# Kernel tuning notes

Measured on AMD Instinct MI355X. Metric: run time of the kernel, lower is better.

## Reference

```python
import jax, jax.numpy as jnp
import numpy as np

B, S, D_MODEL, D_KEY = 4, 2048, 1024, 128


def setup_inputs() -> dict:
    key = jax.random.key(0)
    kq, kk, kv, kwq, kwk, kwv = jax.random.split(key, 6)
    queries = jax.random.normal(kq, (B, S, D_MODEL), dtype=jnp.float32)
    keys = jax.random.normal(kk, (B, S, D_MODEL), dtype=jnp.float32)
    values = jax.random.normal(kv, (B, S, D_MODEL), dtype=jnp.float32)
    # causal mask: 1 where attention is allowed (j <= i), 0 otherwise
    mask = jnp.broadcast_to(jnp.tril(jnp.ones((S, S), dtype=jnp.int32)), (B, S, S))
    # torch nn.Linear weights are [out, in]; init ~ U(-1/sqrt(in), 1/sqrt(in))
    bound = 1.0 / np.sqrt(D_MODEL)
    Wq = jax.random.uniform(kwq, (D_KEY, D_MODEL), jnp.float32, -bound, bound)
    Wk = jax.random.uniform(kwk, (D_KEY, D_MODEL), jnp.float32, -bound, bound)
    Wv = jax.random.uniform(kwv, (D_KEY, D_MODEL), jnp.float32, -bound, bound)
    return {"queries": queries, "keys": keys, "values": values, "mask": mask,
            "Wq": Wq, "Wk": Wk, "Wv": Wv}


def reference(queries, keys, values, mask, Wq, Wk, Wv):
    d_key = Wq.shape[0]
    q = jnp.einsum('bsd,kd->bsk', queries, Wq)   # [B,S,d_key]
    k = jnp.einsum('bsd,kd->bsk', keys, Wk)
    v = jnp.einsum('bsd,kd->bsk', values, Wv)
    attn = jnp.einsum('bqk,bsk->bqs', q, k) / jnp.sqrt(jnp.float32(d_key))  # [B,S,S]
    attn = jnp.where(mask == 0, -jnp.inf, attn)
    attn = jax.nn.softmax(attn, axis=-1)
    return jnp.einsum('bqs,bsk->bqk', attn, v)   # [B,S,d_key]
```

## Files before the change

kernel.cpp:

```cpp
#include <hip/hip_runtime.h>
#include <hip/hip_bf16.h>

#define NB 4
#define SEQ 2048
#define DMODEL 1024
#define DKEY 128

using f32x4  = __attribute__((ext_vector_type(4))) float;
using bf16x8 = __attribute__((ext_vector_type(8))) short;
using u16x4  = __attribute__((ext_vector_type(4))) unsigned short;
using u16x8  = __attribute__((ext_vector_type(8))) unsigned short;

__device__ __forceinline__ unsigned short f2bf(float f) {
  __hip_bfloat16 h = __float2bfloat16(f);
  return __builtin_bit_cast(unsigned short, h);
}
__device__ __forceinline__ bf16x8 pack8(f32x4 lo, f32x4 hi) {
  u16x8 p = { f2bf(lo[0]), f2bf(lo[1]), f2bf(lo[2]), f2bf(lo[3]),
              f2bf(hi[0]), f2bf(hi[1]), f2bf(hi[2]), f2bf(hi[3]) };
  return __builtin_bit_cast(bf16x8, p);
}
__device__ __forceinline__ void gload16(const void* g, void* l) {
  __builtin_amdgcn_global_load_lds(
      (const __attribute__((address_space(1))) void*)g,
      (__attribute__((address_space(3))) void*)l, 16, 0, 0);
}

__global__ __launch_bounds__(256) void wconv_kernel(
    const float* __restrict__ Wq, const float* __restrict__ Wk,
    const float* __restrict__ Wv, unsigned short* __restrict__ Wb)
{
  int id = blockIdx.x * 256 + threadIdx.x;
  const float* src = (id < 16384) ? Wq : (id < 32768) ? Wk : Wv;
  int off = (id & 16383) * 8;
  float4 a = *reinterpret_cast<const float4*>(&src[off]);
  float4 b = *reinterpret_cast<const float4*>(&src[off + 4]);
  u16x8 p = { f2bf(a.x), f2bf(a.y), f2bf(a.z), f2bf(a.w),
              f2bf(b.x), f2bf(b.y), f2bf(b.z), f2bf(b.w) };
  *reinterpret_cast<u16x8*>(&Wb[(size_t)(id >> 14) * 131072 + off]) = p;
}

__global__ __launch_bounds__(256, 2) void proj_kernel(
    const float* __restrict__ Xq, const float* __restrict__ Xk, const float* __restrict__ Xv,
    const unsigned short* __restrict__ Wb,
    unsigned short* __restrict__ Yq, unsigned short* __restrict__ Yk,
    unsigned short* __restrict__ Vt)
{
  const int z = blockIdx.z;
  const float* X = (z == 0) ? Xq : (z == 1) ? Xk : Xv;
  const unsigned short* W = Wb + (size_t)z * 131072;

  __shared__ alignas(16) float          XL[4][64 * 32];
  __shared__ alignas(16) unsigned short WL[4][128 * 32];

  const int t     = threadIdx.x;
  const int lane  = t & 63;
  const int w     = t >> 6;
  const int lr    = lane & 15;
  const int hi    = lane >> 4;
  const int rbase = hi * 4;
  const long m0   = (long)blockIdx.x * 64;

  const int xg_row[2] = { (0 * 256 + t) >> 3, (1 * 256 + t) >> 3 };
  const int xg_col[2] = { ((((0 * 256 + t) & 7) ^ (xg_row[0] & 7)) << 2),
                          ((((1 * 256 + t) & 7) ^ (xg_row[1] & 7)) << 2) };
  const int wg_row[2] = { (0 * 256 + t) >> 2, (1 * 256 + t) >> 2 };
  const int wg_col[2] = { ((((0 * 256 + t) & 3) ^ (wg_row[0] & 3)) << 3),
                          ((((1 * 256 + t) & 3) ^ (wg_row[1] & 3)) << 3) };

#define PJ_ISSUE(ks) do {                                                     \
    const int _b = (ks) & 3;                                                  \
    _Pragma("unroll")                                                         \
    for (int i = 0; i < 2; ++i) {                                             \
      gload16(&X[(m0 + xg_row[i]) * (long)DMODEL + (ks) * 32 + xg_col[i]],    \
              &XL[_b][(i * 256 + w * 64) * 4]);                               \
      gload16(&W[(size_t)wg_row[i] * DMODEL + (ks) * 32 + wg_col[i]],         \
              &WL[_b][(i * 256 + w * 64) * 8]);                               \
    }                                                                         \
  } while (0)

  f32x4 acc[8];
  const f32x4 zero = {0.f, 0.f, 0.f, 0.f};
#pragma unroll
  for (int n = 0; n < 8; ++n) acc[n] = zero;

  PJ_ISSUE(0);
  PJ_ISSUE(1);
  PJ_ISSUE(2);

  const int arow = w * 16 + lr;
  for (int ks = 0; ks < 32; ++ks) {
    if (ks < 30)       asm volatile("s_waitcnt vmcnt(8)" ::: "memory");
    else if (ks == 30) asm volatile("s_waitcnt vmcnt(4)" ::: "memory");
    else               asm volatile("s_waitcnt vmcnt(0)" ::: "memory");
    __builtin_amdgcn_s_barrier();
    if (ks + 3 < 32) PJ_ISSUE(ks + 3);

    const int buf = ks & 3;
    const float* xrow = &XL[buf][arow * 32];
    f32x4 xlo = *reinterpret_cast<const f32x4*>(xrow + (((hi * 2)     ^ (lr & 7)) << 2));
    f32x4 xhi = *reinterpret_cast<const f32x4*>(xrow + (((hi * 2 + 1) ^ (lr & 7)) << 2));
    bf16x8 a = pack8(xlo, xhi);
#pragma unroll
    for (int n = 0; n < 8; ++n) {
      const int wrow = n * 16 + lr;
      bf16x8 b = *reinterpret_cast<const bf16x8*>(
          &WL[buf][wrow * 32 + ((hi ^ (wrow & 3)) << 3)]);
      acc[n] = __builtin_amdgcn_mfma_f32_16x16x32_bf16(a, b, acc[n], 0, 0, 0);
    }
  }
#undef PJ_ISSUE

  if (z != 2) {
    unsigned short* Y = (z == 0) ? Yq : Yk;
#pragma unroll
    for (int n = 0; n < 8; ++n)
#pragma unroll
      for (int r = 0; r < 4; ++r) {
        long row = m0 + w * 16 + rbase + r;
        Y[row * DKEY + n * 16 + lr] = f2bf(acc[n][r]);
      }
  } else {
    unsigned short* Tl = reinterpret_cast<unsigned short*>(&XL[0][0]);
    __syncthreads();
#pragma unroll
    for (int n = 0; n < 8; ++n)
#pragma unroll
      for (int r = 0; r < 4; ++r)
        Tl[(n * 16 + lr) * 72 + (w * 16 + rbase + r)] = f2bf(acc[n][r]);
    __syncthreads();
    const int bb = (int)(m0 >> 11);
    const int s0 = (int)(m0 & 2047);
#pragma unroll
    for (int i = 0; i < 4; ++i) {
      int id = t + 256 * i;
      int dr = id >> 3;
      int c8 = (id & 7) << 3;
      u16x8 v = *reinterpret_cast<const u16x8*>(&Tl[dr * 72 + c8]);
      *reinterpret_cast<u16x8*>(&Vt[((size_t)bb * DKEY + dr) * SEQ + s0 + c8]) = v;
    }
  }
}

__global__ __launch_bounds__(512, 2) void attn_kernel(
    const unsigned short* __restrict__ Q,
    const unsigned short* __restrict__ K,
    const unsigned short* __restrict__ Vt,
    float* __restrict__ O)
{
  const int  L    = blockIdx.x;
  const int  b    = (L & 7) >> 1;
  const int  qt   = 63 - (((L >> 3) << 1) | (L & 1));
  const int  q0   = qt * 32;
  const long base = (long)b * SEQ;
  const int  nt   = (q0 >> 6) + 1;
  const int  nsteps = (nt + 3) >> 2;

  __shared__ alignas(16) unsigned short Kl[4][64][128];
  __shared__ alignas(16) unsigned short Vl[4][128][64];
  __shared__ alignas(16) unsigned short Plds[8][16][72];
  __shared__ float Sm[4][32], Sl[4][32];

  const int t     = threadIdx.x;
  const int lane  = t & 63;
  const int w     = t >> 6;
  const int g     = w >> 1;
  const int wq    = w & 1;
  const int lr    = lane & 15;
  const int hi    = lane >> 4;
  const int lk    = hi * 8;
  const int rbase = hi * 4;

  bf16x8 qa[4];
  {
    const long qrow = (base + q0 + wq * 16 + lr) * (long)DKEY;
#pragma unroll
    for (int dk = 0; dk < 4; ++dk)
      qa[dk] = *reinterpret_cast<const bf16x8*>(&Q[qrow + dk * 32 + lk]);
  }

  const f32x4 zero = {0.f, 0.f, 0.f, 0.f};
  f32x4 oacc[8];
#pragma unroll
  for (int n = 0; n < 8; ++n) oacc[n] = zero;
  float m_run[4], l_run[4];
#pragma unroll
  for (int r = 0; r < 4; ++r) { m_run[r] = -1e30f; l_run[r] = 0.0f; }

  const float sc = 0.08838834764831845f;
  const unsigned short* VtB = Vt + (size_t)b * DKEY * SEQ;

  for (int st = 0; st < nsteps; ++st) {
    const int kt  = st * 4 + g;
    const bool act = kt < nt;
    const int kv0 = kt * 64;

    if (act) {
      const unsigned short* Kp = K + (base + kv0) * (long)DKEY;
#pragma unroll
      for (int it = 0; it < 8; ++it) {
        int c = it * 128 + wq * 64 + lane;
        int row = c >> 4, sl = (c & 15) ^ (row & 7);
        *reinterpret_cast<u16x8*>(&Kl[g][row][sl * 8]) =
            *reinterpret_cast<const u16x8*>(&Kp[(size_t)c * 8]);
      }
#pragma unroll
      for (int it = 0; it < 8; ++it) {
        int c = it * 128 + wq * 64 + lane;
        int d = c >> 3, sl = c & 7, slp = sl ^ (d & 7);
        *reinterpret_cast<u16x8*>(&Vl[g][d][slp * 8]) =
            *reinterpret_cast<const u16x8*>(&VtB[(size_t)d * SEQ + kv0 + sl * 8]);
      }
    }
    __syncthreads();

    if (act) {
      f32x4 s[4];
#pragma unroll
      for (int kc = 0; kc < 4; ++kc) {
        s[kc] = zero;
#pragma unroll
        for (int dk = 0; dk < 4; ++dk) {
          bf16x8 kb = *reinterpret_cast<const bf16x8*>(
              &Kl[g][kc * 16 + lr][((dk * 4 + hi) ^ (lr & 7)) * 8]);
          s[kc] = __builtin_amdgcn_mfma_f32_16x16x32_bf16(qa[dk], kb, s[kc], 0, 0, 0);
        }
      }

      const bool dmask = (kt == nt - 1);
      float x[4][4];
#pragma unroll
      for (int kc = 0; kc < 4; ++kc)
#pragma unroll
        for (int r = 0; r < 4; ++r) {
          float xv = s[kc][r] * sc;
          if (dmask) {
            int col  = kv0 + kc * 16 + lr;
            int rowq = q0 + wq * 16 + rbase + r;
            if (col > rowq) xv = -1e30f;
          }
          x[kc][r] = xv;
        }

#pragma unroll
      for (int r = 0; r < 4; ++r) {
        float tm = fmaxf(fmaxf(x[0][r], x[1][r]), fmaxf(x[2][r], x[3][r]));
        tm = fmaxf(tm, __shfl_xor(tm, 1));
        tm = fmaxf(tm, __shfl_xor(tm, 2));
        tm = fmaxf(tm, __shfl_xor(tm, 4));
        tm = fmaxf(tm, __shfl_xor(tm, 8));
        float mnew = fmaxf(m_run[r], tm);
        float scl  = __expf(m_run[r] - mnew);
        m_run[r] = mnew;
        float ps = 0.0f;
#pragma unroll
        for (int kc = 0; kc < 4; ++kc) {
          float pp = __expf(x[kc][r] - mnew);
          ps += pp;
          Plds[w][rbase + r][kc * 16 + lr] = f2bf(pp);
        }
        ps += __shfl_xor(ps, 1);
        ps += __shfl_xor(ps, 2);
        ps += __shfl_xor(ps, 4);
        ps += __shfl_xor(ps, 8);
        l_run[r] = l_run[r] * scl + ps;
#pragma unroll
        for (int n = 0; n < 8; ++n) oacc[n][r] *= scl;
      }

#pragma unroll
      for (int kk = 0; kk < 2; ++kk) {
        bf16x8 pa = *reinterpret_cast<const bf16x8*>(&Plds[w][lr][kk * 32 + lk]);
#pragma unroll
        for (int n = 0; n < 8; ++n) {
          bf16x8 vb = *reinterpret_cast<const bf16x8*>(
              &Vl[g][n * 16 + lr][((kk * 4 + hi) ^ (lr & 7)) * 8]);
          oacc[n] = __builtin_amdgcn_mfma_f32_16x16x32_bf16(pa, vb, oacc[n], 0, 0, 0);
        }
      }
    }
    __syncthreads();
  }

  float* Om = reinterpret_cast<float*>(&Kl[0][0][0]);
#pragma unroll
  for (int n = 0; n < 8; ++n)
#pragma unroll
    for (int r = 0; r < 4; ++r)
      Om[(g * 32 + wq * 16 + rbase + r) * 128 + n * 16 + lr] = oacc[n][r];
  if (lr == 0) {
#pragma unroll
    for (int r = 0; r < 4; ++r) {
      Sm[g][wq * 16 + rbase + r] = m_run[r];
      Sl[g][wq * 16 + rbase + r] = l_run[r];
    }
  }
  __syncthreads();

  const int row = t >> 4;
  const int c0  = (t & 15) * 8;
  float mM = fmaxf(fmaxf(Sm[0][row], Sm[1][row]), fmaxf(Sm[2][row], Sm[3][row]));
  float wts[4], lsum = 0.0f;
#pragma unroll
  for (int gv = 0; gv < 4; ++gv) {
    wts[gv] = __expf(Sm[gv][row] - mM);
    lsum += wts[gv] * Sl[gv][row];
  }
  const float linv = 1.0f / lsum;
  f32x4 o0 = zero, o1 = zero;
#pragma unroll
  for (int gv = 0; gv < 4; ++gv) {
    const float* src = &Om[(gv * 32 + row) * 128 + c0];
    f32x4 a0 = *reinterpret_cast<const f32x4*>(src);
    f32x4 a1 = *reinterpret_cast<const f32x4*>(src + 4);
    const float wt = wts[gv];
#pragma unroll
    for (int j = 0; j < 4; ++j) { o0[j] += wt * a0[j]; o1[j] += wt * a1[j]; }
  }
#pragma unroll
  for (int j = 0; j < 4; ++j) { o0[j] *= linv; o1[j] *= linv; }
  float* op = &O[(base + q0 + row) * (long)DKEY + c0];
  *reinterpret_cast<f32x4*>(op)     = o0;
  *reinterpret_cast<f32x4*>(op + 4) = o1;
}

extern "C" void kernel_launch(void* const* d_in, const int* in_sizes, int n_in,
                              void* d_out, int out_size, void* d_ws, size_t ws_size,
                              hipStream_t stream) {
  const float* Xq = (const float*)d_in[0];
  const float* Xk = (const float*)d_in[1];
  const float* Xv = (const float*)d_in[2];
  const float* Wq = (const float*)d_in[4];
  const float* Wk = (const float*)d_in[5];
  const float* Wv = (const float*)d_in[6];

  unsigned short* qp  = (unsigned short*)d_ws;
  unsigned short* kp  = qp + (size_t)NB * SEQ * DKEY;
  unsigned short* vtp = kp + (size_t)NB * SEQ * DKEY;
  unsigned short* wbp = (unsigned short*)d_out;

  hipLaunchKernelGGL(wconv_kernel, dim3(192), dim3(256), 0, stream,
                     Wq, Wk, Wv, wbp);
  dim3 g1(SEQ * NB / 64, 1, 3);
  hipLaunchKernelGGL(proj_kernel, g1, dim3(256), 0, stream,
                     Xq, Xk, Xv, wbp, qp, kp, vtp);
  hipLaunchKernelGGL(attn_kernel, dim3(256), dim3(512), 0, stream,
                     qp, kp, vtp, (float*)d_out);
}
```

Before: 68.37 us.

## Stage projection X tile as bf16 in LDS in two halves, double-buffer W

The projection kernel now loads half of the 64-row X tile (512 columns) through registers, converts it to bf16 once, and stores it swizzled in LDS, instead of streaming fp32 X through a 4-deep async global-to-LDS pipeline and converting at every k-step. W keeps async loads but with a 2-stage buffer. This removes the repeated per-step fp32-to-bf16 packing and halves LDS bytes per X element. In exchange, X loads are synchronous bulk phases with no overlap against MFMA work, and an extra barrier is added per step.

```diff
diff --git a/kernel.cpp b/kernel.cpp
--- a/kernel.cpp
+++ b/kernel.cpp
@@ -14,11 +14,6 @@
 __device__ __forceinline__ unsigned short f2bf(float f) {
   __hip_bfloat16 h = __float2bfloat16(f);
   return __builtin_bit_cast(unsigned short, h);
-}
-__device__ __forceinline__ bf16x8 pack8(f32x4 lo, f32x4 hi) {
-  u16x8 p = { f2bf(lo[0]), f2bf(lo[1]), f2bf(lo[2]), f2bf(lo[3]),
-              f2bf(hi[0]), f2bf(hi[1]), f2bf(hi[2]), f2bf(hi[3]) };
-  return __builtin_bit_cast(bf16x8, p);
 }
 __device__ __forceinline__ void gload16(const void* g, void* l) {
   __builtin_amdgcn_global_load_lds(
@@ -50,8 +45,8 @@
   const float* X = (z == 0) ? Xq : (z == 1) ? Xk : Xv;
   const unsigned short* W = Wb + (size_t)z * 131072;
 
-  __shared__ alignas(16) float          XL[4][64 * 32];
-  __shared__ alignas(16) unsigned short WL[4][128 * 32];
+  __shared__ alignas(16) unsigned short XL[64 * 512];
+  __shared__ alignas(16) unsigned short WL[2][128 * 32];
 
   const int t     = threadIdx.x;
   const int lane  = t & 63;
@@ -60,56 +55,81 @@
   const int hi    = lane >> 4;
   const int rbase = hi * 4;
   const long m0   = (long)blockIdx.x * 64;
-
-  const int xg_row[2] = { (0 * 256 + t) >> 3, (1 * 256 + t) >> 3 };
-  const int xg_col[2] = { ((((0 * 256 + t) & 7) ^ (xg_row[0] & 7)) << 2),
-                          ((((1 * 256 + t) & 7) ^ (xg_row[1] & 7)) << 2) };
+  const int arow  = w * 16 + lr;
+
   const int wg_row[2] = { (0 * 256 + t) >> 2, (1 * 256 + t) >> 2 };
   const int wg_col[2] = { ((((0 * 256 + t) & 3) ^ (wg_row[0] & 3)) << 3),
                           ((((1 * 256 + t) & 3) ^ (wg_row[1] & 3)) << 3) };
 
-#define PJ_ISSUE(ks) do {                                                     \
-    const int _b = (ks) & 3;                                                  \
+#define W_ISSUE(ks) do {                                                      \
+    const int _s = (ks) & 1;                                                  \
     _Pragma("unroll")                                                         \
-    for (int i = 0; i < 2; ++i) {                                             \
-      gload16(&X[(m0 + xg_row[i]) * (long)DMODEL + (ks) * 32 + xg_col[i]],    \
-              &XL[_b][(i * 256 + w * 64) * 4]);                               \
+    for (int i = 0; i < 2; ++i)                                               \
       gload16(&W[(size_t)wg_row[i] * DMODEL + (ks) * 32 + wg_col[i]],         \
-              &WL[_b][(i * 256 + w * 64) * 8]);                               \
+              &WL[_s][(i * 256 + w * 64) * 8]);                               \
+  } while (0)
+
+#define P1_LOAD(cbase) do {                                                   \
+    for (int jb = 0; jb < 8; ++jb) {                                          \
+      float4 v[4];                                                            \
+      _Pragma("unroll")                                                       \
+      for (int u = 0; u < 4; ++u) {                                           \
+        int f = (jb * 4 + u) * 256 + t;                                       \
+        int row = f >> 7, c4 = (f & 127) << 2;                                \
+        v[u] = *reinterpret_cast<const float4*>(                              \
+            &X[(m0 + row) * (long)DMODEL + (cbase) + c4]);                    \
+      }                                                                       \
+      _Pragma("unroll")                                                       \
+      for (int u = 0; u < 4; ++u) {                                           \
+        int f = (jb * 4 + u) * 256 + t;                                       \
+        int row = f >> 7, c4 = (f & 127) << 2;                                \
+        u16x4 p = { f2bf(v[u].x), f2bf(v[u].y), f2bf(v[u].z), f2bf(v[u].w) }; \
+        *reinterpret_cast<u16x4*>(                                            \
+            &XL[row * 512 + (((c4 >> 3) ^ (row & 7)) << 3)                    \
+                + ((c4 >> 2) & 1) * 4]) = p;                                  \
+      }                                                                       \
     }                                                                         \
   } while (0)
 
+#define PJ_STEP(gks) do {                                                     \
+    if ((gks) < 31) asm volatile("s_waitcnt vmcnt(2)" ::: "memory");          \
+    else            asm volatile("s_waitcnt vmcnt(0)" ::: "memory");          \
+    __builtin_amdgcn_s_barrier();                                             \
+    {                                                                         \
+      const int _s  = (gks) & 1;                                              \
+      const int _gr = ((gks) & 15) * 4 + hi;                                  \
+      bf16x8 a = *reinterpret_cast<const bf16x8*>(                            \
+          &XL[arow * 512 + ((_gr ^ (lr & 7)) << 3)]);                         \
+      _Pragma("unroll")                                                       \
+      for (int n = 0; n < 8; ++n) {                                           \
+        const int wrow = n * 16 + lr;                                         \
+        bf16x8 b = *reinterpret_cast<const bf16x8*>(                          \
+            &WL[_s][wrow * 32 + ((hi ^ (wrow & 3)) << 3)]);                   \
+        acc[n] = __builtin_amdgcn_mfma_f32_16x16x32_bf16(a, b, acc[n], 0, 0, 0); \
+      }                                                                       \
+    }                                                                         \
+    __builtin_amdgcn_s_barrier();                                             \
+    if ((gks) + 2 < 32) W_ISSUE((gks) + 2);                                   \
+  } while (0)
+
   f32x4 acc[8];
   const f32x4 zero = {0.f, 0.f, 0.f, 0.f};
 #pragma unroll
   for (int n = 0; n < 8; ++n) acc[n] = zero;
 
-  PJ_ISSUE(0);
-  PJ_ISSUE(1);
-  PJ_ISSUE(2);
-
-  const int arow = w * 16 + lr;
-  for (int ks = 0; ks < 32; ++ks) {
-    if (ks < 30)       asm volatile("s_waitcnt vmcnt(8)" ::: "memory");
-    else if (ks == 30) asm volatile("s_waitcnt vmcnt(4)" ::: "memory");
-    else               asm volatile("s_waitcnt vmcnt(0)" ::: "memory");
-    __builtin_amdgcn_s_barrier();
-    if (ks + 3 < 32) PJ_ISSUE(ks + 3);
-
-    const int buf = ks & 3;
-    const float* xrow = &XL[buf][arow * 32];
-    f32x4 xlo = *reinterpret_cast<const f32x4*>(xrow + (((hi * 2)     ^ (lr & 7)) << 2));
-    f32x4 xhi = *reinterpret_cast<const f32x4*>(xrow + (((hi * 2 + 1) ^ (lr & 7)) << 2));
-    bf16x8 a = pack8(xlo, xhi);
-#pragma unroll
-    for (int n = 0; n < 8; ++n) {
-      const int wrow = n * 16 + lr;
-      bf16x8 b = *reinterpret_cast<const bf16x8*>(
-          &WL[buf][wrow * 32 + ((hi ^ (wrow & 3)) << 3)]);
-      acc[n] = __builtin_amdgcn_mfma_f32_16x16x32_bf16(a, b, acc[n], 0, 0, 0);
-    }
-  }
-#undef PJ_ISSUE
+  P1_LOAD(0);
+  __syncthreads();
+  W_ISSUE(0);
+  W_ISSUE(1);
+  for (int ks = 0; ks < 16; ++ks) PJ_STEP(ks);
+
+  P1_LOAD(512);
+  __syncthreads();
+  for (int ks = 16; ks < 32; ++ks) PJ_STEP(ks);
+
+#undef W_ISSUE
+#undef P1_LOAD
+#undef PJ_STEP
 
   if (z != 2) {
     unsigned short* Y = (z == 0) ? Yq : Yk;
@@ -121,7 +141,7 @@
         Y[row * DKEY + n * 16 + lr] = f2bf(acc[n][r]);
       }
   } else {
-    unsigned short* Tl = reinterpret_cast<unsigned short*>(&XL[0][0]);
+    unsigned short* Tl = XL;
     __syncthreads();
 #pragma unroll
     for (int n = 0; n < 8; ++n)
```

Result: slower. 70.76 us (+3.5%).
